# Kernel optimization log

Measured on AMD Instinct MI355X. Metric: run time of the kernel, lower is better.

Reference implementation:

```python
import jax, jax.numpy as jnp
import numpy as np
import math

D_MODEL = 1024
N_HEAD = 16
HEAD_DIM = D_MODEL // N_HEAD


def setup_inputs() -> dict:
    key = jax.random.key(0)
    ks = jax.random.split(key, 9)
    B, S = 2, 2048
    x = jax.random.normal(ks[0], (B, S, D_MODEL), dtype=jnp.float32)
    # nn.Linear weights are [out, in]; default-ish init scale 0.02, phase projs std=0.005
    w = lambda k, std: jax.random.normal(k, (D_MODEL, D_MODEL), dtype=jnp.float32) * std
    return {
        "x": x,
        "Wq_amp": w(ks[1], 0.02),
        "Wk_amp": w(ks[2], 0.02),
        "Wq_phi": w(ks[3], 0.005),
        "Wk_phi": w(ks[4], 0.005),
        "Wv": w(ks[5], 0.02),
        "Wo": w(ks[6], 0.02),
        "score_log_scale": jnp.zeros((N_HEAD,), dtype=jnp.float32),
    }


def _split_heads(t):
    B, S, _ = t.shape
    return t.reshape(B, S, N_HEAD, HEAD_DIM).transpose(0, 2, 1, 3)  # [B,H,S,hd]


def reference(x, Wq_amp, Wk_amp, Wq_phi, Wk_phi, Wv, Wo, score_log_scale):
    B, S, _ = x.shape
    eps = 1e-6
    # amplitude (softplus) and phase (pi * tanh) projections
    q_amp = _split_heads(jax.nn.softplus(x @ Wq_amp.T))
    k_amp = _split_heads(jax.nn.softplus(x @ Wk_amp.T))
    q_phi = _split_heads(math.pi * jnp.tanh(x @ Wq_phi.T))
    k_phi = _split_heads(math.pi * jnp.tanh(x @ Wk_phi.T))
    # RMS-normalize amplitudes over head_dim
    q_amp = q_amp / jnp.sqrt(jnp.mean(q_amp * q_amp, axis=-1, keepdims=True) + eps)
    k_amp = k_amp / jnp.sqrt(jnp.mean(k_amp * k_amp, axis=-1, keepdims=True) + eps)
    # interference components
    q_cos = q_amp * jnp.cos(q_phi)
    q_sin = q_amp * jnp.sin(q_phi)
    k_cos = k_amp * jnp.cos(k_phi)
    k_sin = k_amp * jnp.sin(k_phi)
    # two-term score matmul, scaled
    scores = (jnp.einsum("bhqd,bhkd->bhqk", q_cos, k_cos)
              + jnp.einsum("bhqd,bhkd->bhqk", q_sin, k_sin)) / math.sqrt(HEAD_DIM)
    scores = scores * jnp.exp(score_log_scale)[None, :, None, None]
    # causal mask + softmax
    mask = jnp.tril(jnp.ones((S, S), dtype=bool))
    scores = jnp.where(mask[None, None], scores, -jnp.inf)
    attn = jax.nn.softmax(scores, axis=-1)
    v = _split_heads(x @ Wv.T)
    out = jnp.einsum("bhqk,bhkd->bhqd", attn, v)
    out = out.transpose(0, 2, 1, 3).reshape(B, S, D_MODEL)
    return out @ Wo.T
```

## Files before the change

### kernel.cpp

```cpp
#include <hip/hip_runtime.h>
#include <hip/hip_bf16.h>
#include <math.h>

#define S_LEN 2048
#define NH 16
#define HD 64
#define DM 1024
#define NTOK 4096
#define NBH 32

typedef __attribute__((ext_vector_type(8))) __bf16 bf16x8;
typedef __attribute__((ext_vector_type(8))) ushort ushort8;
typedef __attribute__((ext_vector_type(4))) ushort ushort4v;
typedef __attribute__((ext_vector_type(4))) float f32x4;
typedef __attribute__((ext_vector_type(16))) float f32x16;
typedef __attribute__((ext_vector_type(4))) uint u32x4;

__device__ __forceinline__ ushort f2b(float x) {
  __hip_bfloat16 h = __float2bfloat16(x);
  return *reinterpret_cast<ushort*>(&h);
}

__device__ __forceinline__ uint pk2(float lo, float hi) {
  return (uint)f2b(lo) | ((uint)f2b(hi) << 16);
}

__device__ __forceinline__ void gload16b(const void* g, void* l) {
  __builtin_amdgcn_global_load_lds((const __attribute__((address_space(1))) void*)g,
                                   (__attribute__((address_space(3))) void*)l, 16, 0, 0);
}

#define MFMA16(a, b, c) __builtin_amdgcn_mfma_f32_16x16x32_bf16((a), (b), (c), 0, 0, 0)
#define MFMA32(a, b, c) __builtin_amdgcn_mfma_f32_32x32x16_bf16((a), (b), (c), 0, 0, 0)

struct CvtArgs {
  const float* src[7];
  ushort* dst[7];
  int n[7];
};

__global__ void cvt_kernel(CvtArgs a) {
  int arr = blockIdx.y;
  long i = ((long)blockIdx.x * blockDim.x + threadIdx.x) * 8;
  if (i >= a.n[arr]) return;
  const float* s = a.src[arr];
  ushort* d = a.dst[arr];
  float4 v0 = *reinterpret_cast<const float4*>(s + i);
  float4 v1 = *reinterpret_cast<const float4*>(s + i + 4);
  ushort8 r;
  r[0] = f2b(v0.x); r[1] = f2b(v0.y); r[2] = f2b(v0.z); r[3] = f2b(v0.w);
  r[4] = f2b(v1.x); r[5] = f2b(v1.y); r[6] = f2b(v1.z); r[7] = f2b(v1.w);
  *reinterpret_cast<ushort8*>(d + i) = r;
}

__global__ __launch_bounds__(256, 2) void qkproj_kernel(
    const ushort* __restrict__ A,
    const ushort* __restrict__ Wqa, const ushort* __restrict__ Wqp,
    const ushort* __restrict__ Wka, const ushort* __restrict__ Wkp,
    const ushort* __restrict__ Wv, const float* __restrict__ sls,
    ushort* __restrict__ qext, ushort* __restrict__ kext, ushort* __restrict__ vT) {
  __shared__ __align__(16) ushort Alds[3][4096];
  __shared__ __align__(16) ushort B0lds[3][4096];
  __shared__ __align__(16) ushort B1lds[3][4096];
  const int d = blockIdx.x;
  const int xc = d & 7, c = d >> 3;
  const int u = (c < 64) ? (xc * 64 + c) : (512 + xc * 32 + (c - 64));
  int z, bx, by;
  if (u < 512) { z = u >> 8; int v = u & 255; bx = v & 7; by = v >> 3; }
  else         { z = 2;      int v = u - 512; bx = v & 7; by = v >> 3; }
  const int t = threadIdx.x;
  const int lane = t & 63;
  const int wave = t >> 6;
  const int wm = wave >> 1, wn = wave & 1;
  const int l15 = lane & 15, g = lane >> 4;
  const int mbase = by * 128, nbase = bx * 128;
  const int K = DM;
  const int srow = t >> 2;
  const int sx = (srow >> 1) & 3;
  const int scol = (((t & 3) ^ sx)) * 8;
  const int xr = (l15 >> 1) & 3;
  const ushort* Ag = A + (size_t)(mbase + srow) * K + scol;
  const ushort* Wa = (z == 0) ? Wqa : (z == 1) ? Wka : Wv;
  const ushort* Wp = (z == 0) ? Wqp : Wkp;
  const ushort* Wag = Wa + (size_t)(nbase + srow) * K + scol;
  const ushort* Wpg = (z < 2) ? (Wp + (size_t)(nbase + srow) * K + scol) : Wag;

  const int nk = K / 32;
  f32x4 accA[4][4] = {};

  if (z < 2) {
    f32x4 accP[4][4] = {};
    auto stage = [&](int buf, int kt) {
      gload16b(Ag + kt, &Alds[buf][t * 8]);
      gload16b(Ag + kt + (size_t)64 * K, &Alds[buf][t * 8 + 64 * 32]);
      gload16b(Wag + kt, &B0lds[buf][t * 8]);
      gload16b(Wag + kt + (size_t)64 * K, &B0lds[buf][t * 8 + 64 * 32]);
      gload16b(Wpg + kt, &B1lds[buf][t * 8]);
      gload16b(Wpg + kt + (size_t)64 * K, &B1lds[buf][t * 8 + 64 * 32]);
    };
    stage(0, 0);
    stage(1, 32);
    int cur = 0;
    for (int kt = 0; kt < nk; ++kt) {
      if (kt + 2 < nk) {
        int b2 = cur + 2; if (b2 >= 3) b2 -= 3;
        stage(b2, (kt + 2) * 32);
        asm volatile("s_waitcnt vmcnt(12)" ::: "memory");
      } else if (kt + 1 < nk) {
        asm volatile("s_waitcnt vmcnt(6)" ::: "memory");
      } else {
        asm volatile("s_waitcnt vmcnt(0)" ::: "memory");
      }
      __builtin_amdgcn_s_barrier();
      bf16x8 af[4], ba[4], bp[4];
#pragma unroll
      for (int i = 0; i < 4; i++)
        af[i] = *reinterpret_cast<const bf16x8*>(
            &Alds[cur][(wm * 64 + i * 16 + l15) * 32 + (g ^ xr) * 8]);
#pragma unroll
      for (int j = 0; j < 4; j++) {
        ba[j] = *reinterpret_cast<const bf16x8*>(
            &B0lds[cur][(wn * 64 + j * 16 + l15) * 32 + (g ^ xr) * 8]);
        bp[j] = *reinterpret_cast<const bf16x8*>(
            &B1lds[cur][(wn * 64 + j * 16 + l15) * 32 + (g ^ xr) * 8]);
      }
      __builtin_amdgcn_s_setprio(1);
#pragma unroll
      for (int i = 0; i < 4; i++)
#pragma unroll
        for (int j = 0; j < 4; j++) {
          accA[i][j] = MFMA16(af[i], ba[j], accA[i][j]);
          accP[i][j] = MFMA16(af[i], bp[j], accP[i][j]);
        }
      __builtin_amdgcn_s_setprio(0);
      __builtin_amdgcn_s_barrier();
      cur = (cur + 1 == 3) ? 0 : cur + 1;
    }
    const int row0 = mbase + wm * 64;
    const int h = (nbase >> 6) + wn;
    const float scale = (z == 0) ? __expf(sls[h]) * 0.125f : 1.0f;
    ushort* ext = (z == 0) ? qext : kext;
#pragma unroll
    for (int i = 0; i < 4; i++) {
#pragma unroll
      for (int r = 0; r < 4; r++) {
        float sp[4];
        float ss = 0.0f;
#pragma unroll
        for (int j = 0; j < 4; j++) {
          float v = accA[i][j][r];
          sp[j] = fmaxf(v, 0.0f) + __logf(1.0f + __expf(-fabsf(v)));
          ss += sp[j] * sp[j];
        }
        ss += __shfl_xor(ss, 1);
        ss += __shfl_xor(ss, 2);
        ss += __shfl_xor(ss, 4);
        ss += __shfl_xor(ss, 8);
        float rn = rsqrtf(ss * (1.0f / 64.0f) + 1e-6f) * scale;
        const int token = row0 + i * 16 + g * 4 + r;
        const int bb = token >> 11, sidx = token & 2047;
        ushort* base = ext + (((size_t)(bb * NH + h) * S_LEN + sidx) << 7);
#pragma unroll
        for (int j = 0; j < 4; j++) {
          float e = __expf(2.0f * accP[i][j][r]);
          float th = 1.0f - 2.0f * __builtin_amdgcn_rcpf(e + 1.0f);
          float phi = 3.14159265358979f * th;
          float sn = __sinf(phi), cs = __cosf(phi);
          float a = sp[j] * rn;
          int dd = j * 16 + l15;
          base[dd] = f2b(a * cs);
          base[64 + dd] = f2b(a * sn);
        }
      }
    }
  } else {
    auto stage = [&](int buf, int kt) {
      gload16b(Ag + kt, &Alds[buf][t * 8]);
      gload16b(Ag + kt + (size_t)64 * K, &Alds[buf][t * 8 + 64 * 32]);
      gload16b(Wag + kt, &B0lds[buf][t * 8]);
      gload16b(Wag + kt + (size_t)64 * K, &B0lds[buf][t * 8 + 64 * 32]);
    };
    stage(0, 0);
    stage(1, 32);
    int cur = 0;
    for (int kt = 0; kt < nk; ++kt) {
      if (kt + 2 < nk) {
        int b2 = cur + 2; if (b2 >= 3) b2 -= 3;
        stage(b2, (kt + 2) * 32);
        asm volatile("s_waitcnt vmcnt(8)" ::: "memory");
      } else if (kt + 1 < nk) {
        asm volatile("s_waitcnt vmcnt(4)" ::: "memory");
      } else {
        asm volatile("s_waitcnt vmcnt(0)" ::: "memory");
      }
      __builtin_amdgcn_s_barrier();
      bf16x8 af[4], ba[4];
#pragma unroll
      for (int i = 0; i < 4; i++)
        af[i] = *reinterpret_cast<const bf16x8*>(
            &Alds[cur][(wm * 64 + i * 16 + l15) * 32 + (g ^ xr) * 8]);
#pragma unroll
      for (int j = 0; j < 4; j++)
        ba[j] = *reinterpret_cast<const bf16x8*>(
            &B0lds[cur][(wn * 64 + j * 16 + l15) * 32 + (g ^ xr) * 8]);
      __builtin_amdgcn_s_setprio(1);
#pragma unroll
      for (int i = 0; i < 4; i++)
#pragma unroll
        for (int j = 0; j < 4; j++)
          accA[i][j] = MFMA16(af[i], ba[j], accA[i][j]);
      __builtin_amdgcn_s_setprio(0);
      __builtin_amdgcn_s_barrier();
      cur = (cur + 1 == 3) ? 0 : cur + 1;
    }
    const int row0 = mbase + wm * 64, col0 = nbase + wn * 64;
#pragma unroll
    for (int i = 0; i < 4; i++)
#pragma unroll
      for (int j = 0; j < 4; j++) {
        int col = col0 + j * 16 + l15;
        int h = col >> 6, hd = col & 63;
        int t0 = row0 + i * 16 + g * 4;
        int bb = t0 >> 11, s0 = t0 & 2047;
        ushort4v w;
#pragma unroll
        for (int r = 0; r < 4; r++) w[r] = f2b(accA[i][j][r]);
        *reinterpret_cast<ushort4v*>(
            &vT[(((size_t)(bb * NH + h) * HD + hd) << 11) + s0]) = w;
      }
  }
}

__global__ __launch_bounds__(256) void gemm_bt(const ushort* __restrict__ A,
                                               const ushort* __restrict__ W,
                                               float* __restrict__ Cout,
                                               int M, int N, int K) {
  __shared__ __align__(16) ushort Alds[4][4096];
  __shared__ __align__(16) ushort Blds[4][4096];
  const int d = blockIdx.x;
  const int u = (d & 7) * 32 + (d >> 3);
  const int bx = u & 7, by = u >> 3;
  const int t = threadIdx.x;
  const int lane = t & 63;
  const int wave = t >> 6;
  const int wm = wave >> 1, wn = wave & 1;
  const int l15 = lane & 15, g = lane >> 4;
  const int mbase = by * 128, nbase = bx * 128;
  const int srow = t >> 2;
  const int sx = (srow >> 1) & 3;
  const int scol = (((t & 3) ^ sx)) * 8;
  const int xr = (l15 >> 1) & 3;
  const ushort* Ag = A + (size_t)(mbase + srow) * K + scol;
  const ushort* Wg = W + (size_t)(nbase + srow) * K + scol;
  auto stage = [&](int buf, int kt) {
    gload16b(Ag + kt, &Alds[buf][t * 8]);
    gload16b(Ag + kt + (size_t)64 * K, &Alds[buf][t * 8 + 64 * 32]);
    gload16b(Wg + kt, &Blds[buf][t * 8]);
    gload16b(Wg + kt + (size_t)64 * K, &Blds[buf][t * 8 + 64 * 32]);
  };
  const int nk = K / 32;
  stage(0, 0);
  stage(1, 32);
  stage(2, 64);
  f32x4 acc[4][4] = {};
  for (int kt = 0; kt < nk; ++kt) {
    const int cur = kt & 3;
    if (kt + 3 < nk) {
      stage((cur + 3) & 3, (kt + 3) * 32);
      asm volatile("s_waitcnt vmcnt(12)" ::: "memory");
    } else if (kt + 2 < nk) {
      asm volatile("s_waitcnt vmcnt(8)" ::: "memory");
    } else if (kt + 1 < nk) {
      asm volatile("s_waitcnt vmcnt(4)" ::: "memory");
    } else {
      asm volatile("s_waitcnt vmcnt(0)" ::: "memory");
    }
    __builtin_amdgcn_s_barrier();
    bf16x8 af[4], bfr[4];
#pragma unroll
    for (int i = 0; i < 4; i++)
      af[i] = *reinterpret_cast<const bf16x8*>(
          &Alds[cur][(wm * 64 + i * 16 + l15) * 32 + (g ^ xr) * 8]);
#pragma unroll
    for (int j = 0; j < 4; j++)
      bfr[j] = *reinterpret_cast<const bf16x8*>(
          &Blds[cur][(wn * 64 + j * 16 + l15) * 32 + (g ^ xr) * 8]);
    __builtin_amdgcn_s_setprio(1);
#pragma unroll
    for (int i = 0; i < 4; i++)
#pragma unroll
      for (int j = 0; j < 4; j++)
        acc[i][j] = MFMA16(af[i], bfr[j], acc[i][j]);
    __builtin_amdgcn_s_setprio(0);
    __builtin_amdgcn_s_barrier();
  }
  const int row0 = mbase + wm * 64, col0 = nbase + wn * 64;
#pragma unroll
  for (int i = 0; i < 4; i++)
#pragma unroll
    for (int j = 0; j < 4; j++)
#pragma unroll
      for (int r = 0; r < 4; r++) {
        int row = row0 + i * 16 + g * 4 + r;
        int col = col0 + j * 16 + l15;
        Cout[(size_t)row * N + col] = acc[i][j][r];
      }
}

__device__ __forceinline__ void stage_kv(const char* Kp, const char* Vp, int kb,
                                         char* buf, int wave, int lane) {
#pragma unroll
  for (int c = 0; c < 4; c++) {
    int i = wave * 4 + c;
    int kvl = i * 4 + (lane >> 4);
    int slot = (lane & 15) ^ (kvl & 7);
    gload16b(Kp + (size_t)(kb + kvl) * 256 + slot * 16, buf + i * 1024);
  }
#pragma unroll
  for (int c = 0; c < 2; c++) {
    int i = wave * 2 + c;
    int hd = i * 8 + (lane >> 3);
    int slot = (lane & 7) ^ (hd & 7);
    gload16b(Vp + (size_t)hd * (S_LEN * 2) + (size_t)kb * 2 + slot * 16,
             buf + 16384 + i * 1024);
  }
}

__global__ __launch_bounds__(256, 3) void attn_kernel(const ushort* __restrict__ qext,
                                                      const ushort* __restrict__ kext,
                                                      const ushort* __restrict__ vT,
                                                      ushort* __restrict__ attnout,
                                                      float* __restrict__ part) {
  __shared__ __align__(16) char lds[2][24576];
  const int d = blockIdx.x;
  const int xcd = d & 7, c = d >> 3;
  const int bh = xcd * 4 + (c & 3);
  const int w = c >> 2;
  int qt, t0, t1, half;
  bool split;
  if (w < 8) { qt = w; t0 = 0; t1 = 2 * qt + 1; split = false; half = 0; }
  else {
    int ww = w - 8;
    qt = 8 + (ww >> 1); half = ww & 1; split = true;
    if (half == 0) { t0 = 0; t1 = qt; } else { t0 = qt + 1; t1 = 2 * qt + 1; }
  }
  const int b = bh >> 4, h = bh & 15;
  const int wave = threadIdx.x >> 6, lane = threadIdx.x & 63;
  const int l31 = lane & 31, hi = lane >> 5;
  const int qb = qt * 128;
  const int qw = qb + wave * 32;
  const int qa = qw + l31;
  const char* Kp = (const char*)(kext + (size_t)bh * S_LEN * 128);
  const char* Vp = (const char*)(vT + (size_t)bh * HD * S_LEN);
  const ushort* Qp = qext + (size_t)bh * S_LEN * 128;
  const int ksw = l31 & 7;

  stage_kv(Kp, Vp, t0 << 6, lds[0], wave, lane);
  bf16x8 qf[8];
#pragma unroll
  for (int s = 0; s < 8; s++)
    qf[s] = *reinterpret_cast<const bf16x8*>(&Qp[(size_t)qa * 128 + s * 16 + hi * 8]);

  f32x16 o0 = {}, o1 = {};
  float m = -1e30f, ls = 0.0f;

  for (int t = t0; t <= t1; ++t) {
    const int cur = (t - t0) & 1;
    const int kb = t << 6;
    if (t < t1) {
      stage_kv(Kp, Vp, (t + 1) << 6, lds[cur ^ 1], wave, lane);
      asm volatile("s_waitcnt vmcnt(6)" ::: "memory");
    } else {
      asm volatile("s_waitcnt vmcnt(0)" ::: "memory");
    }
    __builtin_amdgcn_s_barrier();

    const char* Kb = lds[cur];
    const char* Vb = lds[cur] + 16384;

    f32x16 st0 = {}, st1 = {};
    __builtin_amdgcn_s_setprio(1);
#pragma unroll
    for (int s = 0; s < 8; s++) {
      int sl = ((s * 2 + hi) ^ ksw) << 4;
      bf16x8 k0 = *(const bf16x8*)(Kb + l31 * 256 + sl);
      bf16x8 k1 = *(const bf16x8*)(Kb + (32 + l31) * 256 + sl);
      st0 = MFMA32(k0, qf[s], st0);
      st1 = MFMA32(k1, qf[s], st1);
    }
    __builtin_amdgcn_s_setprio(0);

    if (kb + 64 > qw) {
#pragma unroll
      for (int r = 0; r < 16; r++) {
        int kv = kb + (r & 3) + 8 * (r >> 2) + 4 * hi;
        if (kv > qa) st0[r] = -1e30f;
        if (kv + 32 > qa) st1[r] = -1e30f;
      }
    }
    float pm = -1e30f;
#pragma unroll
    for (int r = 0; r < 16; r++) pm = fmaxf(pm, fmaxf(st0[r], st1[r]));
    pm = fmaxf(pm, __shfl_xor(pm, 32));
    if (!__all(pm <= m + 8.0f)) {
      float mn = fmaxf(m, pm);
      float corr = __expf(m - mn);
      m = mn;
      ls *= corr;
#pragma unroll
      for (int r = 0; r < 16; r++) { o0[r] *= corr; o1[r] *= corr; }
    }
    float ssum = 0.0f;
#pragma unroll
    for (int r = 0; r < 16; r++) {
      st0[r] = __expf(st0[r] - m);
      st1[r] = __expf(st1[r] - m);
      ssum += st0[r] + st1[r];
    }
    ssum += __shfl_xor(ssum, 32);
    ls += ssum;

    u32x4 pb[4];
#pragma unroll
    for (int hf = 0; hf < 2; hf++) {
      const f32x16& st = hf ? st1 : st0;
      uint cA0 = pk2(st[0], st[1]),  cA1 = pk2(st[2], st[3]);
      uint cB0 = pk2(st[4], st[5]),  cB1 = pk2(st[6], st[7]);
      uint cC0 = pk2(st[8], st[9]),  cC1 = pk2(st[10], st[11]);
      uint cD0 = pk2(st[12], st[13]), cD1 = pk2(st[14], st[15]);
      uint xA0 = __shfl_xor(cA0, 32), xA1 = __shfl_xor(cA1, 32);
      uint xB0 = __shfl_xor(cB0, 32), xB1 = __shfl_xor(cB1, 32);
      uint xC0 = __shfl_xor(cC0, 32), xC1 = __shfl_xor(cC1, 32);
      uint xD0 = __shfl_xor(cD0, 32), xD1 = __shfl_xor(cD1, 32);
      u32x4 lo, hi4;
      lo[0] = cA0; lo[1] = cA1; lo[2] = xA0; lo[3] = xA1;
      hi4[0] = xB0; hi4[1] = xB1; hi4[2] = cB0; hi4[3] = cB1;
      pb[hf * 2] = hi ? hi4 : lo;
      u32x4 lo2, hi2;
      lo2[0] = cC0; lo2[1] = cC1; lo2[2] = xC0; lo2[3] = xC1;
      hi2[0] = xD0; hi2[1] = xD1; hi2[2] = cD0; hi2[3] = cD1;
      pb[hf * 2 + 1] = hi ? hi2 : lo2;
    }
    __builtin_amdgcn_s_setprio(1);
#pragma unroll
    for (int ks = 0; ks < 4; ks++) {
      int sl = ((ks * 2 + hi) ^ ksw) << 4;
      bf16x8 v0 = *(const bf16x8*)(Vb + l31 * 128 + sl);
      bf16x8 v1 = *(const bf16x8*)(Vb + (32 + l31) * 128 + sl);
      bf16x8 pbb = *reinterpret_cast<const bf16x8*>(&pb[ks]);
      o0 = MFMA32(v0, pbb, o0);
      o1 = MFMA32(v1, pbb, o1);
    }
    __builtin_amdgcn_s_setprio(0);
    __builtin_amdgcn_s_barrier();
  }

  if (!split) {
    float inv = 1.0f / ls;
    ushort* Op = attnout + ((size_t)b * S_LEN + qa) * DM + h * HD;
#pragma unroll
    for (int g4 = 0; g4 < 4; g4++) {
      ushort4v w0, w1;
#pragma unroll
      for (int jj = 0; jj < 4; jj++) {
        w0[jj] = f2b(o0[4 * g4 + jj] * inv);
        w1[jj] = f2b(o1[4 * g4 + jj] * inv);
      }
      *reinterpret_cast<ushort4v*>(Op + 8 * g4 + 4 * hi) = w0;
      *reinterpret_cast<ushort4v*>(Op + 32 + 8 * g4 + 4 * hi) = w1;
    }
  } else {
    float* P = part + ((size_t)(half * 256 + bh * 8 + (qt - 8)) * 128
                       + (wave * 32 + l31)) * 72;
#pragma unroll
    for (int g4 = 0; g4 < 4; g4++) {
      float4 a0 = make_float4(o0[4 * g4], o0[4 * g4 + 1], o0[4 * g4 + 2], o0[4 * g4 + 3]);
      float4 a1 = make_float4(o1[4 * g4], o1[4 * g4 + 1], o1[4 * g4 + 2], o1[4 * g4 + 3]);
      *reinterpret_cast<float4*>(P + 8 * g4 + 4 * hi) = a0;
      *reinterpret_cast<float4*>(P + 32 + 8 * g4 + 4 * hi) = a1;
    }
    if (hi == 0) { P[64] = m; P[65] = ls; }
  }
}

__global__ void attn_merge(const float* __restrict__ part, ushort* __restrict__ attnout) {
  const int blk = blockIdx.x;
  const int row = threadIdx.x;
  const int bh = blk >> 3, qt = (blk & 7) + 8;
  const float* Pa = part + ((size_t)blk * 128 + row) * 72;
  const float* Pb = part + ((size_t)(256 + blk) * 128 + row) * 72;
  float mA = Pa[64], lsA = Pa[65], mB = Pb[64], lsB = Pb[65];
  float M = fmaxf(mA, mB);
  float ca = __expf(mA - M), cb = __expf(mB - M);
  float inv = 1.0f / (lsA * ca + lsB * cb);
  const int b = bh >> 4, h = bh & 15;
  const int q = qt * 128 + row;
  ushort* Op = attnout + ((size_t)b * S_LEN + q) * DM + h * HD;
#pragma unroll
  for (int dd = 0; dd < 64; dd += 4) {
    float4 va = *reinterpret_cast<const float4*>(Pa + dd);
    float4 vb = *reinterpret_cast<const float4*>(Pb + dd);
    ushort4v wv;
    wv[0] = f2b((va.x * ca + vb.x * cb) * inv);
    wv[1] = f2b((va.y * ca + vb.y * cb) * inv);
    wv[2] = f2b((va.z * ca + vb.z * cb) * inv);
    wv[3] = f2b((va.w * ca + vb.w * cb) * inv);
    *reinterpret_cast<ushort4v*>(Op + dd) = wv;
  }
}

extern "C" void kernel_launch(void* const* d_in, const int* in_sizes, int n_in,
                              void* d_out, int out_size, void* d_ws, size_t ws_size,
                              hipStream_t stream) {
  const float* x   = (const float*)d_in[0];
  const float* Wqa = (const float*)d_in[1];
  const float* Wka = (const float*)d_in[2];
  const float* Wqp = (const float*)d_in[3];
  const float* Wkp = (const float*)d_in[4];
  const float* Wv  = (const float*)d_in[5];
  const float* Wo  = (const float*)d_in[6];
  const float* sls = (const float*)d_in[7];

  char* ws = (char*)d_ws;
  ushort* x_bf = (ushort*)ws; ws += (size_t)NTOK * DM * 2;
  ushort* w_bf[6];
  for (int i = 0; i < 6; i++) { w_bf[i] = (ushort*)ws; ws += (size_t)DM * DM * 2; }
  ushort* qext = (ushort*)ws; ws += (size_t)NBH * S_LEN * 128 * 2;
  ushort* kext = (ushort*)ws; ws += (size_t)NBH * S_LEN * 128 * 2;
  ushort* vT   = (ushort*)ws; ws += (size_t)NBH * HD * S_LEN * 2;
  ushort* attn = (ushort*)ws; ws += (size_t)NTOK * DM * 2;
  float* part  = (float*)ws;  ws += (size_t)2 * 256 * 128 * 72 * 4;

  CvtArgs ca;
  ca.src[0] = x; ca.dst[0] = x_bf; ca.n[0] = NTOK * DM;
  const float* wsrc[6] = {Wqa, Wka, Wqp, Wkp, Wv, Wo};
  for (int i = 0; i < 6; i++) { ca.src[i + 1] = wsrc[i]; ca.dst[i + 1] = w_bf[i]; ca.n[i + 1] = DM * DM; }
  dim3 cg((NTOK * DM / 8 + 255) / 256, 7);
  hipLaunchKernelGGL(cvt_kernel, cg, dim3(256), 0, stream, ca);

  hipLaunchKernelGGL(qkproj_kernel, dim3(768), dim3(256), 0, stream,
                     x_bf, w_bf[0], w_bf[2], w_bf[1], w_bf[3], w_bf[4], sls,
                     qext, kext, vT);

  hipLaunchKernelGGL(attn_kernel, dim3(768), dim3(256), 0, stream,
                     qext, kext, vT, attn, part);
  hipLaunchKernelGGL(attn_merge, dim3(256), dim3(128), 0, stream, part, attn);

  hipLaunchKernelGGL(gemm_bt, dim3(256), dim3(256), 0, stream, attn, w_bf[5],
                     (float*)d_out, NTOK, DM, DM);
}
```

Before: 155.9 us.

## Enlarge QKV projection tiles to 256x128 with 512 threads and K=64 stages

The fused Q/K/V projection kernel now uses 256-row tiles with 8 waves, a 64-wide K step, and double buffering instead of triple buffering, with stage prefetch issued after the compute barrier. The grid is halved to 384 blocks with a new tile-to-block mapping and an 8-way XOR swizzle for the wider LDS rows. The bf16 conversion kernel becomes grid-strided with a fixed 512x7 grid, cutting the launch count for the large activation array. The aim is better operand reuse and fewer loop iterations, at the cost of higher LDS use per block (about 128KB), which may reduce occupancy and latency hiding.

```diff
diff --git a/kernel.cpp b/kernel.cpp
--- a/kernel.cpp
+++ b/kernel.cpp
@@ -41,103 +41,100 @@
 
 __global__ void cvt_kernel(CvtArgs a) {
   int arr = blockIdx.y;
-  long i = ((long)blockIdx.x * blockDim.x + threadIdx.x) * 8;
-  if (i >= a.n[arr]) return;
   const float* s = a.src[arr];
   ushort* d = a.dst[arr];
-  float4 v0 = *reinterpret_cast<const float4*>(s + i);
-  float4 v1 = *reinterpret_cast<const float4*>(s + i + 4);
-  ushort8 r;
-  r[0] = f2b(v0.x); r[1] = f2b(v0.y); r[2] = f2b(v0.z); r[3] = f2b(v0.w);
-  r[4] = f2b(v1.x); r[5] = f2b(v1.y); r[6] = f2b(v1.z); r[7] = f2b(v1.w);
-  *reinterpret_cast<ushort8*>(d + i) = r;
-}
-
-__global__ __launch_bounds__(256, 2) void qkproj_kernel(
+  long n = a.n[arr];
+  for (long i = ((long)blockIdx.x * 256 + threadIdx.x) * 8; i < n; i += 512L * 256 * 8) {
+    float4 v0 = *reinterpret_cast<const float4*>(s + i);
+    float4 v1 = *reinterpret_cast<const float4*>(s + i + 4);
+    ushort8 r;
+    r[0] = f2b(v0.x); r[1] = f2b(v0.y); r[2] = f2b(v0.z); r[3] = f2b(v0.w);
+    r[4] = f2b(v1.x); r[5] = f2b(v1.y); r[6] = f2b(v1.z); r[7] = f2b(v1.w);
+    *reinterpret_cast<ushort8*>(d + i) = r;
+  }
+}
+
+__global__ __launch_bounds__(512, 2) void qkproj_kernel(
     const ushort* __restrict__ A,
     const ushort* __restrict__ Wqa, const ushort* __restrict__ Wqp,
     const ushort* __restrict__ Wka, const ushort* __restrict__ Wkp,
     const ushort* __restrict__ Wv, const float* __restrict__ sls,
     ushort* __restrict__ qext, ushort* __restrict__ kext, ushort* __restrict__ vT) {
-  __shared__ __align__(16) ushort Alds[3][4096];
-  __shared__ __align__(16) ushort B0lds[3][4096];
-  __shared__ __align__(16) ushort B1lds[3][4096];
-  const int d = blockIdx.x;
-  const int xc = d & 7, c = d >> 3;
-  const int u = (c < 64) ? (xc * 64 + c) : (512 + xc * 32 + (c - 64));
+  __shared__ __align__(16) ushort Alds[2][256 * 64];
+  __shared__ __align__(16) ushort B0lds[2][128 * 64];
+  __shared__ __align__(16) ushort B1lds[2][128 * 64];
+  const int dd0 = blockIdx.x;
+  const int xc = dd0 & 7, c0 = dd0 >> 3;
   int z, bx, by;
-  if (u < 512) { z = u >> 8; int v = u & 255; bx = v & 7; by = v >> 3; }
-  else         { z = 2;      int v = u - 512; bx = v & 7; by = v >> 3; }
+  if (c0 < 32) { int u = xc * 32 + c0; z = u >> 7; int r = u & 127; bx = r & 7; by = r >> 3; }
+  else         { int u = xc * 16 + (c0 - 32); z = 2; bx = u & 7; by = u >> 3; }
   const int t = threadIdx.x;
   const int lane = t & 63;
   const int wave = t >> 6;
   const int wm = wave >> 1, wn = wave & 1;
   const int l15 = lane & 15, g = lane >> 4;
-  const int mbase = by * 128, nbase = bx * 128;
+  const int mbase = by * 256, nbase = bx * 128;
   const int K = DM;
-  const int srow = t >> 2;
-  const int sx = (srow >> 1) & 3;
-  const int scol = (((t & 3) ^ sx)) * 8;
-  const int xr = (l15 >> 1) & 3;
+  const int srow = t >> 3;
+  const int sx = (t >> 4) & 7;
+  const int scol = ((t & 7) ^ sx) * 8;
+  const int xr = l15 >> 1;
   const ushort* Ag = A + (size_t)(mbase + srow) * K + scol;
   const ushort* Wa = (z == 0) ? Wqa : (z == 1) ? Wka : Wv;
   const ushort* Wp = (z == 0) ? Wqp : Wkp;
   const ushort* Wag = Wa + (size_t)(nbase + srow) * K + scol;
   const ushort* Wpg = (z < 2) ? (Wp + (size_t)(nbase + srow) * K + scol) : Wag;
-
-  const int nk = K / 32;
-  f32x4 accA[4][4] = {};
+  const int nk = K / 64;
 
   if (z < 2) {
-    f32x4 accP[4][4] = {};
+    f32x4 accA[4][4] = {}, accP[4][4] = {};
     auto stage = [&](int buf, int kt) {
-      gload16b(Ag + kt, &Alds[buf][t * 8]);
-      gload16b(Ag + kt + (size_t)64 * K, &Alds[buf][t * 8 + 64 * 32]);
-      gload16b(Wag + kt, &B0lds[buf][t * 8]);
-      gload16b(Wag + kt + (size_t)64 * K, &B0lds[buf][t * 8 + 64 * 32]);
-      gload16b(Wpg + kt, &B1lds[buf][t * 8]);
-      gload16b(Wpg + kt + (size_t)64 * K, &B1lds[buf][t * 8 + 64 * 32]);
+      const int kb = kt * 64;
+#pragma unroll
+      for (int c = 0; c < 4; c++)
+        gload16b(Ag + kb + (size_t)(c * 64) * K, &Alds[buf][(c * 512 + t) * 8]);
+#pragma unroll
+      for (int c = 0; c < 2; c++) {
+        gload16b(Wag + kb + (size_t)(c * 64) * K, &B0lds[buf][(c * 512 + t) * 8]);
+        gload16b(Wpg + kb + (size_t)(c * 64) * K, &B1lds[buf][(c * 512 + t) * 8]);
+      }
     };
     stage(0, 0);
-    stage(1, 32);
-    int cur = 0;
+    stage(1, 1);
     for (int kt = 0; kt < nk; ++kt) {
-      if (kt + 2 < nk) {
-        int b2 = cur + 2; if (b2 >= 3) b2 -= 3;
-        stage(b2, (kt + 2) * 32);
-        asm volatile("s_waitcnt vmcnt(12)" ::: "memory");
-      } else if (kt + 1 < nk) {
-        asm volatile("s_waitcnt vmcnt(6)" ::: "memory");
-      } else {
-        asm volatile("s_waitcnt vmcnt(0)" ::: "memory");
-      }
+      const int cur = kt & 1;
+      if (kt < nk - 1) asm volatile("s_waitcnt vmcnt(8)" ::: "memory");
+      else             asm volatile("s_waitcnt vmcnt(0)" ::: "memory");
       __builtin_amdgcn_s_barrier();
-      bf16x8 af[4], ba[4], bp[4];
-#pragma unroll
-      for (int i = 0; i < 4; i++)
-        af[i] = *reinterpret_cast<const bf16x8*>(
-            &Alds[cur][(wm * 64 + i * 16 + l15) * 32 + (g ^ xr) * 8]);
-#pragma unroll
-      for (int j = 0; j < 4; j++) {
-        ba[j] = *reinterpret_cast<const bf16x8*>(
-            &B0lds[cur][(wn * 64 + j * 16 + l15) * 32 + (g ^ xr) * 8]);
-        bp[j] = *reinterpret_cast<const bf16x8*>(
-            &B1lds[cur][(wn * 64 + j * 16 + l15) * 32 + (g ^ xr) * 8]);
-      }
-      __builtin_amdgcn_s_setprio(1);
-#pragma unroll
-      for (int i = 0; i < 4; i++)
+#pragma unroll
+      for (int kk = 0; kk < 2; kk++) {
+        bf16x8 af[4], b0[4], b1[4];
+#pragma unroll
+        for (int i = 0; i < 4; i++)
+          af[i] = *reinterpret_cast<const bf16x8*>(
+              &Alds[cur][(wm * 64 + i * 16 + l15) * 64 + ((kk * 4 + g) ^ xr) * 8]);
 #pragma unroll
         for (int j = 0; j < 4; j++) {
-          accA[i][j] = MFMA16(af[i], ba[j], accA[i][j]);
-          accP[i][j] = MFMA16(af[i], bp[j], accP[i][j]);
+          b0[j] = *reinterpret_cast<const bf16x8*>(
+              &B0lds[cur][(wn * 64 + j * 16 + l15) * 64 + ((kk * 4 + g) ^ xr) * 8]);
+          b1[j] = *reinterpret_cast<const bf16x8*>(
+              &B1lds[cur][(wn * 64 + j * 16 + l15) * 64 + ((kk * 4 + g) ^ xr) * 8]);
         }
-      __builtin_amdgcn_s_setprio(0);
+        __builtin_amdgcn_s_setprio(1);
+#pragma unroll
+        for (int i = 0; i < 4; i++)
+#pragma unroll
+          for (int j = 0; j < 4; j++) {
+            accA[i][j] = MFMA16(af[i], b0[j], accA[i][j]);
+            accP[i][j] = MFMA16(af[i], b1[j], accP[i][j]);
+          }
+        __builtin_amdgcn_s_setprio(0);
+      }
       __builtin_amdgcn_s_barrier();
-      cur = (cur + 1 == 3) ? 0 : cur + 1;
+      if (kt + 2 < nk) stage(cur, kt + 2);
     }
     const int row0 = mbase + wm * 64;
-    const int h = (nbase >> 6) + wn;
+    const int h = bx * 2 + wn;
     const float scale = (z == 0) ? __expf(sls[h]) * 0.125f : 1.0f;
     ushort* ext = (z == 0) ? qext : kext;
 #pragma unroll
@@ -167,51 +164,51 @@
           float phi = 3.14159265358979f * th;
           float sn = __sinf(phi), cs = __cosf(phi);
           float a = sp[j] * rn;
-          int dd = j * 16 + l15;
-          base[dd] = f2b(a * cs);
-          base[64 + dd] = f2b(a * sn);
+          int dc = j * 16 + l15;
+          base[dc] = f2b(a * cs);
+          base[64 + dc] = f2b(a * sn);
         }
       }
     }
   } else {
+    f32x4 acc[4][4] = {};
     auto stage = [&](int buf, int kt) {
-      gload16b(Ag + kt, &Alds[buf][t * 8]);
-      gload16b(Ag + kt + (size_t)64 * K, &Alds[buf][t * 8 + 64 * 32]);
-      gload16b(Wag + kt, &B0lds[buf][t * 8]);
-      gload16b(Wag + kt + (size_t)64 * K, &B0lds[buf][t * 8 + 64 * 32]);
+      const int kb = kt * 64;
+#pragma unroll
+      for (int c = 0; c < 4; c++)
+        gload16b(Ag + kb + (size_t)(c * 64) * K, &Alds[buf][(c * 512 + t) * 8]);
+#pragma unroll
+      for (int c = 0; c < 2; c++)
+        gload16b(Wag + kb + (size_t)(c * 64) * K, &B0lds[buf][(c * 512 + t) * 8]);
     };
     stage(0, 0);
-    stage(1, 32);
-    int cur = 0;
+    stage(1, 1);
     for (int kt = 0; kt < nk; ++kt) {
-      if (kt + 2 < nk) {
-        int b2 = cur + 2; if (b2 >= 3) b2 -= 3;
-        stage(b2, (kt + 2) * 32);
-        asm volatile("s_waitcnt vmcnt(8)" ::: "memory");
-      } else if (kt + 1 < nk) {
-        asm volatile("s_waitcnt vmcnt(4)" ::: "memory");
-      } else {
-        asm volatile("s_waitcnt vmcnt(0)" ::: "memory");
-      }
+      const int cur = kt & 1;
+      if (kt < nk - 1) asm volatile("s_waitcnt vmcnt(6)" ::: "memory");
+      else             asm volatile("s_waitcnt vmcnt(0)" ::: "memory");
       __builtin_amdgcn_s_barrier();
-      bf16x8 af[4], ba[4];
-#pragma unroll
-      for (int i = 0; i < 4; i++)
-        af[i] = *reinterpret_cast<const bf16x8*>(
-            &Alds[cur][(wm * 64 + i * 16 + l15) * 32 + (g ^ xr) * 8]);
-#pragma unroll
-      for (int j = 0; j < 4; j++)
-        ba[j] = *reinterpret_cast<const bf16x8*>(
-            &B0lds[cur][(wn * 64 + j * 16 + l15) * 32 + (g ^ xr) * 8]);
-      __builtin_amdgcn_s_setprio(1);
-#pragma unroll
-      for (int i = 0; i < 4; i++)
+#pragma unroll
+      for (int kk = 0; kk < 2; kk++) {
+        bf16x8 af[4], bv[4];
+#pragma unroll
+        for (int i = 0; i < 4; i++)
+          af[i] = *reinterpret_cast<const bf16x8*>(
+              &Alds[cur][(wm * 64 + i * 16 + l15) * 64 + ((kk * 4 + g) ^ xr) * 8]);
 #pragma unroll
         for (int j = 0; j < 4; j++)
-          accA[i][j] = MFMA16(af[i], ba[j], accA[i][j]);
-      __builtin_amdgcn_s_setprio(0);
+          bv[j] = *reinterpret_cast<const bf16x8*>(
+              &B0lds[cur][(wn * 64 + j * 16 + l15) * 64 + ((kk * 4 + g) ^ xr) * 8]);
+        __builtin_amdgcn_s_setprio(1);
+#pragma unroll
+        for (int i = 0; i < 4; i++)
+#pragma unroll
+          for (int j = 0; j < 4; j++)
+            acc[i][j] = MFMA16(af[i], bv[j], acc[i][j]);
+        __builtin_amdgcn_s_setprio(0);
+      }
       __builtin_amdgcn_s_barrier();
-      cur = (cur + 1 == 3) ? 0 : cur + 1;
+      if (kt + 2 < nk) stage(cur, kt + 2);
     }
     const int row0 = mbase + wm * 64, col0 = nbase + wn * 64;
 #pragma unroll
@@ -224,7 +221,7 @@
         int bb = t0 >> 11, s0 = t0 & 2047;
         ushort4v w;
 #pragma unroll
-        for (int r = 0; r < 4; r++) w[r] = f2b(accA[i][j][r]);
+        for (int r = 0; r < 4; r++) w[r] = f2b(acc[i][j][r]);
         *reinterpret_cast<ushort4v*>(
             &vT[(((size_t)(bb * NH + h) * HD + hd) << 11) + s0]) = w;
       }
@@ -535,10 +532,9 @@
   ca.src[0] = x; ca.dst[0] = x_bf; ca.n[0] = NTOK * DM;
   const float* wsrc[6] = {Wqa, Wka, Wqp, Wkp, Wv, Wo};
   for (int i = 0; i < 6; i++) { ca.src[i + 1] = wsrc[i]; ca.dst[i + 1] = w_bf[i]; ca.n[i + 1] = DM * DM; }
-  dim3 cg((NTOK * DM / 8 + 255) / 256, 7);
-  hipLaunchKernelGGL(cvt_kernel, cg, dim3(256), 0, stream, ca);
-
-  hipLaunchKernelGGL(qkproj_kernel, dim3(768), dim3(256), 0, stream,
+  hipLaunchKernelGGL(cvt_kernel, dim3(512, 7), dim3(256), 0, stream, ca);
+
+  hipLaunchKernelGGL(qkproj_kernel, dim3(384), dim3(512), 0, stream,
                      x_bf, w_bf[0], w_bf[2], w_bf[1], w_bf[3], w_bf[4], sls,
                      qext, kext, vT);
 
```

After: 160.2 us. 1.03x slower.
